# Kernel optimization log

Hardware: AMD Instinct MI355X
Metric: run time of the kernel (lower is better)

Reference implementation:

```python
import jax, jax.numpy as jnp
import numpy as np

B, N, E, S, HOPS, OD = 32, 325, 64, 12, 3, 1


def setup_inputs() -> dict:
    key = jax.random.key(0)
    ks = jax.random.split(key, 16)
    rn = lambda k, sh: jax.random.normal(k, sh, dtype=jnp.float32)
    return {
        "hidden": rn(ks[0], (B, N, E)),
        "supports": jax.random.uniform(ks[1], (2, N, N), dtype=jnp.float32),
        "target": rn(ks[2], (B, S, N, OD)),
        "memory": rn(ks[3], (HOPS + 1, B, N, E)),
        "nodevec1": rn(ks[4], (N, E)),
        "nodevec2": rn(ks[5], (N, E)),
        "gru_w_ih": rn(ks[6], (3 * E, OD)) * 0.1,
        "gru_w_hh": rn(ks[7], (3 * E, E)) * 0.1,
        "gru_b_ih": rn(ks[8], (3 * E,)) * 0.1,
        "gru_b_hh": rn(ks[9], (3 * E,)) * 0.1,
        "sent_w": rn(ks[10], (HOPS, E, E)) * 0.1,  # sentinel Linear (no bias), stored pre-transposed
        "bn_gamma": jnp.ones((HOPS, N), dtype=jnp.float32),
        "bn_beta": jnp.zeros((HOPS, N), dtype=jnp.float32),
        "gconv_w": rn(ks[11], (HOPS, 7 * E, E)) * 0.05,  # order*support_len+1 = 7 chunks
        "gconv_b": rn(ks[12], (HOPS, E)) * 0.05,
        "out_w": rn(ks[13], (E, OD)) * 0.1,
        "out_b": rn(ks[14], (OD,)) * 0.1,
    }


def _bn(x, gamma, beta, eps=1e-5):
    # nn.BatchNorm1d(num_nodes) on (B, N, E): channel dim is N, stats over (B, E) (training-mode batch stats)
    mean = x.mean(axis=(0, 2), keepdims=True)
    var = x.var(axis=(0, 2), keepdims=True)
    return (x - mean) / jnp.sqrt(var + eps) * gamma[None, :, None] + beta[None, :, None]


def _gconv(x, sup_list, score, W, b):
    # order=2, support_len=3 -> 1 + 2*3 = 7 concatenated chunks, then Linear(7E -> E)
    outs = [x]
    for adj in sup_list:
        x1 = jnp.einsum('nm,bme->bne', adj, x)
        outs.append(jnp.einsum('bnm,bme->bne', score, x1))
        x2 = jnp.einsum('nm,bme->bne', adj, x1)
        outs.append(jnp.einsum('bnm,bme->bne', score, x2))
    return jnp.concatenate(outs, axis=-1) @ W + b


def reference(hidden, supports, target, memory, nodevec1, nodevec2,
              gru_w_ih, gru_w_hh, gru_b_ih, gru_b_hh, sent_w,
              bn_gamma, bn_beta, gconv_w, gconv_b, out_w, out_b):
    Bn, Nn, Ee = hidden.shape
    scale = Ee ** 0.5
    adp = jax.nn.softmax(jax.nn.relu(nodevec1 @ nodevec2.T), axis=-1)
    sup_list = [supports[0], supports[1], adp]

    def step(carry, _):
        h, prev = carry  # h: (B,N,E), prev: (B,N,OD) previous prediction (zeros at t=0)
        gi = prev.reshape(Bn * Nn, -1) @ gru_w_ih.T + gru_b_ih
        gh = h.reshape(Bn * Nn, Ee) @ gru_w_hh.T + gru_b_hh
        i_r, i_z, i_n = jnp.split(gi, 3, axis=-1)
        h_r, h_z, h_n = jnp.split(gh, 3, axis=-1)
        r = jax.nn.sigmoid(i_r + h_r)
        z = jax.nn.sigmoid(i_z + h_z)
        n = jnp.tanh(i_n + r * h_n)
        h_new = ((1.0 - z) * n + z * h.reshape(Bn * Nn, Ee)).reshape(Bn, Nn, Ee)
        u = h_new
        sents, mems = [], []
        for hop in range(HOPS):
            key_m = memory[hop]  # (B,N,E)
            energy = jnp.einsum('bne,bme->bnm', u, key_m) / scale  # (B,N,N)
            sent = jnp.sum(u * (key_m @ sent_w[hop]), axis=-1) / scale  # (B,N)
            sents.append(sent)
            score = jax.nn.softmax(energy, axis=-1)
            o = _bn(_gconv(memory[hop + 1], sup_list, score, gconv_w[hop], gconv_b[hop]),
                    bn_gamma[hop], bn_beta[hop])
            mems.append(o)
            u = u + o
        sents = jnp.stack(sents, axis=-1)   # (B,N,hops)
        mems = jnp.stack(mems, axis=-2)     # (B,N,hops,E)
        # NOTE: original code weights with RAW sentinel energies, not sentinel_score (dead code) -- kept faithful
        out = jnp.sum(sents[..., None] * mems, axis=-2) @ out_w + out_b  # (B,N,OD)
        return (h_new, out), out

    init_out = jnp.zeros((Bn, Nn, OD), dtype=hidden.dtype)
    _, outs = jax.lax.scan(step, (hidden, init_out), None, length=S)  # (S,B,N,OD)
    return jnp.transpose(outs, (1, 0, 2, 3))  # (B,S,N,OD)
```

## Files before the change

### kernel.cpp

```cpp
#include <hip/hip_runtime.h>

constexpr int B = 32, N = 325, E = 64, S = 12, HOPS = 3;
constexpr int BN  = B * N;
constexpr int BNE = B * N * E;
constexpr int RT  = 16;
constexpr int NRT = (N + RT - 1) / RT;
constexpr int EP  = E + 4;
constexpr int NP  = 328;
constexpr int PSTR = 348;
constexpr int PBSTR = 360;
constexpr float SCALE_INV = 0.125f;

typedef __attribute__((ext_vector_type(8))) short short8v;
typedef __attribute__((ext_vector_type(4))) float f32x4;

__device__ inline short f2bf(float f) {
  unsigned x = __builtin_bit_cast(unsigned, f);
  return (short)((x + 0x7FFFu + ((x >> 16) & 1u)) >> 16);
}
__device__ inline float bf2f(short h) {
  unsigned x = ((unsigned)(unsigned short)h) << 16;
  return __builtin_bit_cast(float, x);
}

__global__ __launch_bounds__(256) void adp_kernel(const float* __restrict__ nv1,
                                                  const float* __restrict__ nv2,
                                                  float* __restrict__ adp) {
  int n = blockIdx.x;
  __shared__ float row[E];
  __shared__ float buf[N];
  __shared__ float red[256];
  int tid = threadIdx.x;
  if (tid < E) row[tid] = nv1[n * E + tid];
  __syncthreads();
  float lmax = -1e30f;
  for (int m = tid; m < N; m += 256) {
    const float* v2 = nv2 + (size_t)m * E;
    float s = 0.f;
#pragma unroll
    for (int e = 0; e < E; ++e) s += row[e] * v2[e];
    s = fmaxf(s, 0.f);
    buf[m] = s;
    lmax = fmaxf(lmax, s);
  }
  red[tid] = lmax;
  __syncthreads();
  for (int off = 128; off > 0; off >>= 1) {
    if (tid < off) red[tid] = fmaxf(red[tid], red[tid + off]);
    __syncthreads();
  }
  float mx = red[0];
  __syncthreads();
  float lsum = 0.f;
  for (int m = tid; m < N; m += 256) {
    float ev = expf(buf[m] - mx);
    buf[m] = ev;
    lsum += ev;
  }
  red[tid] = lsum;
  __syncthreads();
  for (int off = 128; off > 0; off >>= 1) {
    if (tid < off) red[tid] += red[tid + off];
    __syncthreads();
  }
  float inv = 1.f / red[0];
  for (int m = tid; m < N; m += 256) adp[(size_t)n * N + m] = buf[m] * inv;
}

__device__ inline void rowmm_body(const float* __restrict__ in, const float* __restrict__ W,
                                  const float* __restrict__ bias, float* __restrict__ out,
                                  int accum, int blk, int nblk) {
  __shared__ float Wl[E][E + 1];
  __shared__ float rbuf[4][4][E];
  int tid = threadIdx.x, w = tid >> 6, l = tid & 63;
  for (int idx = tid; idx < E * E; idx += 256) Wl[idx >> 6][idx & 63] = W[idx];
  __syncthreads();
  float bv = bias ? bias[l] : 0.f;
  constexpr int NG = BN / 16;
  for (int g = blk; g < NG; g += nblk) {
    int base = g * 16 + w * 4;
#pragma unroll
    for (int rr = 0; rr < 4; ++rr) rbuf[w][rr][l] = in[(size_t)(base + rr) * E + l];
    float acc[4];
#pragma unroll
    for (int rr = 0; rr < 4; ++rr)
      acc[rr] = accum ? out[(size_t)(base + rr) * E + l] : bv;
#pragma unroll
    for (int k = 0; k < 16; ++k) {
      float w0 = Wl[4 * k][l], w1 = Wl[4 * k + 1][l], w2 = Wl[4 * k + 2][l], w3 = Wl[4 * k + 3][l];
#pragma unroll
      for (int rr = 0; rr < 4; ++rr) {
        float4 rv = *(const float4*)&rbuf[w][rr][4 * k];
        acc[rr] += rv.x * w0 + rv.y * w1 + rv.z * w2 + rv.w * w3;
      }
    }
#pragma unroll
    for (int rr = 0; rr < 4; ++rr) out[(size_t)(base + rr) * E + l] = acc[rr];
  }
}

__global__ __launch_bounds__(256) void rowmmA_kernel(const float* __restrict__ memory,
                                                     const float* __restrict__ sent_w,
                                                     const float* __restrict__ gw,
                                                     const float* __restrict__ gb,
                                                     float* __restrict__ kms,
                                                     float* __restrict__ C0) {
  int c = blockIdx.x / 112, blk = blockIdx.x % 112;
  const float *in, *W, *bias;
  float* out;
  if (c < 3) {
    in = memory + (size_t)c * BNE; W = sent_w + (size_t)c * E * E; bias = nullptr;
    out = kms + (size_t)c * BNE;
  } else {
    int h = c - 3;
    in = memory + (size_t)(h + 1) * BNE; W = gw + (size_t)h * 7 * E * E; bias = gb + h * E;
    out = C0 + (size_t)h * BNE;
  }
  rowmm_body(in, W, bias, out, 0, blk, 112);
}

__global__ __launch_bounds__(256) void rowmmZ_kernel(const float* __restrict__ tbase,
                                                     const float* __restrict__ gw,
                                                     int chunk, float* __restrict__ Zb,
                                                     int accum) {
  int h = blockIdx.x / 224, blk = blockIdx.x % 224;
  rowmm_body(tbase + (size_t)h * BNE, gw + (size_t)h * 7 * E * E + (size_t)chunk * E * E,
             nullptr, Zb + (size_t)h * BNE, accum, blk, 224);
}

__global__ __launch_bounds__(256) void bmmB_kernel(const float* __restrict__ A,
                                                   const float* __restrict__ Xbase,
                                                   float* __restrict__ outBase) {
  int c = blockIdx.x / (B * NRT), rem = blockIdx.x % (B * NRT);
  int b = rem / NRT, rt = rem % NRT;
  const float* X = Xbase + (size_t)c * BNE;
  float* out = outBase + (size_t)c * BNE;
  int n0 = rt * RT, nrows = min(RT, N - n0);
  __shared__ float Ar[RT][NP];
  __shared__ float tile[64][EP];
  int tid = threadIdx.x, w = tid >> 6, l = tid & 63;
  for (int r = w; r < RT; r += 4)
    for (int m = l; m < NP; m += 64)
      Ar[r][m] = (r < nrows && m < N) ? A[(size_t)(n0 + r) * N + m] : 0.f;
  int ti = tid >> 2, c0 = (tid & 3) * 16;
  float acc[4] = {0.f, 0.f, 0.f, 0.f};
  for (int mt = 0; mt < 6; ++mt) {
    int m0 = mt * 64, mv = min(64, N - m0);
    __syncthreads();
    {
      float4 z0, z1, z2, z3;
      if (ti < mv) {
        const float4* src = (const float4*)(X + ((size_t)b * N + m0 + ti) * E + c0);
        z0 = src[0]; z1 = src[1]; z2 = src[2]; z3 = src[3];
      } else {
        z0 = z1 = z2 = z3 = make_float4(0.f, 0.f, 0.f, 0.f);
      }
      float4* dst = (float4*)&tile[ti][c0];
      dst[0] = z0; dst[1] = z1; dst[2] = z2; dst[3] = z3;
    }
    __syncthreads();
    int jmax = (mv + 3) >> 2;
#pragma unroll 4
    for (int j = 0; j < jmax; ++j) {
      float t0 = tile[4 * j][l], t1 = tile[4 * j + 1][l];
      float t2 = tile[4 * j + 2][l], t3 = tile[4 * j + 3][l];
#pragma unroll
      for (int rr = 0; rr < 4; ++rr) {
        float4 p = *(const float4*)&Ar[w * 4 + rr][m0 + 4 * j];
        acc[rr] += p.x * t0 + p.y * t1 + p.z * t2 + p.w * t3;
      }
    }
  }
#pragma unroll
  for (int rr = 0; rr < 4; ++rr) {
    int r = w * 4 + rr;
    if (r < nrows) out[((size_t)b * N + n0 + r) * E + l] = acc[rr];
  }
}

__global__ __launch_bounds__(128) void kpack_kernel(const float* __restrict__ memory,
                                                    short* __restrict__ kp) {
  int idx = blockIdx.x;
  int ct = idx % 21, hb = idx / 21;
  int tid = threadIdx.x, ks = tid >> 6, l = tid & 63;
  int m = ct * 16 + (l & 15);
  int e0 = ks * 32 + (l >> 4) * 8;
  short8v hi, lo;
  if (m < N) {
    const float* p = memory + ((size_t)hb * N + m) * E + e0;
#pragma unroll
    for (int j = 0; j < 8; ++j) {
      float f = p[j];
      short h = f2bf(f);
      hi[j] = h;
      lo[j] = f2bf(f - bf2f(h));
    }
  } else {
#pragma unroll
    for (int j = 0; j < 8; ++j) { hi[j] = 0; lo[j] = 0; }
  }
  size_t base = ((size_t)idx * 2 + ks) * 1024 + (size_t)l * 8;
  *(short8v*)(kp + base) = hi;
  *(short8v*)(kp + base + 512) = lo;
}

__global__ __launch_bounds__(64) void zpack_kernel(const float* __restrict__ Zb,
                                                   short* __restrict__ zp) {
  int idx = blockIdx.x;
  int et = idx & 3, hb = idx >> 2;
  int l = threadIdx.x;
  int e = et * 16 + (l & 15);
  int mbase = (l >> 4) * 8;
  const float* Zp = Zb + (size_t)hb * N * E;
  for (int ks = 0; ks < 11; ++ks) {
    short8v hi, lo;
#pragma unroll
    for (int j = 0; j < 8; ++j) {
      int m = ks * 32 + mbase + j;
      float f = (m < N) ? Zp[(size_t)m * E + e] : 0.f;
      short h = f2bf(f);
      hi[j] = h;
      lo[j] = f2bf(f - bf2f(h));
    }
    size_t base = ((size_t)idx * 11 + ks) * 1024 + (size_t)l * 8;
    *(short8v*)(zp + base) = hi;
    *(short8v*)(zp + base + 512) = lo;
  }
}

__global__ __launch_bounds__(256) void attn_kernel(
    const float* __restrict__ uPrev, const float* __restrict__ gprePrev,
    const float* __restrict__ statsPrev, const float* __restrict__ gammaPrev,
    const float* __restrict__ betaPrev, const float* __restrict__ outw,
    float* __restrict__ uOut, float* __restrict__ owPrev,
    const float* __restrict__ kms, const short* __restrict__ kp,
    const short* __restrict__ zp, const float* __restrict__ C0,
    float* __restrict__ gpre, float* __restrict__ statsCur,
    float* __restrict__ sent) {
  int b = blockIdx.x / 11, rt = blockIdx.x % 11;
  int n0 = rt * 32, nrows = min(32, N - n0);
  int tid = threadIdx.x, w = tid >> 6, l = tid & 63;
  __shared__ float uT[32][68];
  __shared__ float prob[32][PSTR];
  __shared__ short pb[32][PBSTR];
  __shared__ float rsum[32];
  size_t rowbase = (size_t)b * N + n0;

  for (int rr = 0; rr < 8; ++rr) {
    int r = w * 8 + rr;
    if (r < nrows) {
      size_t gi = (rowbase + r) * E + l;
      float uv;
      if (gprePrev) {
        int n = n0 + r;
        float m = statsPrev[n] * (1.f / 2048.f);
        float var = statsPrev[N + n] * (1.f / 2048.f) - m * m;
        float rstd = rsqrtf(var + 1e-5f);
        float o = (gprePrev[gi] - m) * rstd * gammaPrev[n] + betaPrev[n];
        uv = uPrev[gi] + o;
        if (uOut) uOut[gi] = uv;
        float tt = o * outw[l];
#pragma unroll
        for (int off = 32; off; off >>= 1) tt += __shfl_xor(tt, off);
        if (l == 0) owPrev[rowbase + r] = tt;
      } else {
        uv = uPrev[gi];
      }
      uT[r][l] = uv;
    } else if (r < 32) uT[r][l] = 0.f;
  }
  __syncthreads();
  for (int rr = 0; rr < 8; ++rr) {
    int r = w * 8 + rr;
    if (r < nrows) {
      float v = uT[r][l] * kms[(rowbase + r) * E + l];
#pragma unroll
      for (int off = 32; off; off >>= 1) v += __shfl_xor(v, off);
      if (l == 0) sent[rowbase + r] = v * SCALE_INV;
    }
  }
  short8v ah[2][2], al[2][2];
  {
    int arow = l & 15, ak = (l >> 4) * 8;
#pragma unroll
    for (int mt = 0; mt < 2; ++mt)
#pragma unroll
      for (int ks = 0; ks < 2; ++ks) {
        const float* p = &uT[mt * 16 + arow][ks * 32 + ak];
        short8v h, lo;
#pragma unroll
        for (int j = 0; j < 8; ++j) {
          float f = p[j];
          short hh = f2bf(f);
          h[j] = hh;
          lo[j] = f2bf(f - bf2f(hh));
        }
        ah[mt][ks] = h; al[mt][ks] = lo;
      }
  }
  const short8v* kpb = (const short8v*)(kp + (size_t)b * 21 * 2048);
  for (int ct = w; ct < 21; ct += 4) {
    short8v bh0 = kpb[(ct * 4 + 0) * 64 + l];
    short8v bl0 = kpb[(ct * 4 + 1) * 64 + l];
    short8v bh1 = kpb[(ct * 4 + 2) * 64 + l];
    short8v bl1 = kpb[(ct * 4 + 3) * 64 + l];
    f32x4 acc0 = {0.f, 0.f, 0.f, 0.f}, acc1 = {0.f, 0.f, 0.f, 0.f};
    acc0 = __builtin_amdgcn_mfma_f32_16x16x32_bf16(ah[0][0], bh0, acc0, 0, 0, 0);
    acc0 = __builtin_amdgcn_mfma_f32_16x16x32_bf16(ah[0][0], bl0, acc0, 0, 0, 0);
    acc0 = __builtin_amdgcn_mfma_f32_16x16x32_bf16(al[0][0], bh0, acc0, 0, 0, 0);
    acc0 = __builtin_amdgcn_mfma_f32_16x16x32_bf16(ah[0][1], bh1, acc0, 0, 0, 0);
    acc0 = __builtin_amdgcn_mfma_f32_16x16x32_bf16(ah[0][1], bl1, acc0, 0, 0, 0);
    acc0 = __builtin_amdgcn_mfma_f32_16x16x32_bf16(al[0][1], bh1, acc0, 0, 0, 0);
    acc1 = __builtin_amdgcn_mfma_f32_16x16x32_bf16(ah[1][0], bh0, acc1, 0, 0, 0);
    acc1 = __builtin_amdgcn_mfma_f32_16x16x32_bf16(ah[1][0], bl0, acc1, 0, 0, 0);
    acc1 = __builtin_amdgcn_mfma_f32_16x16x32_bf16(al[1][0], bh0, acc1, 0, 0, 0);
    acc1 = __builtin_amdgcn_mfma_f32_16x16x32_bf16(ah[1][1], bh1, acc1, 0, 0, 0);
    acc1 = __builtin_amdgcn_mfma_f32_16x16x32_bf16(ah[1][1], bl1, acc1, 0, 0, 0);
    acc1 = __builtin_amdgcn_mfma_f32_16x16x32_bf16(al[1][1], bh1, acc1, 0, 0, 0);
    int col = ct * 16 + (l & 15), r0 = (l >> 4) * 4;
#pragma unroll
    for (int r = 0; r < 4; ++r) {
      prob[r0 + r][col] = acc0[r] * SCALE_INV;
      prob[16 + r0 + r][col] = acc1[r] * SCALE_INV;
    }
  }
  __syncthreads();
  for (int rr = 0; rr < 8; ++rr) {
    int r = w * 8 + rr;
    if (r < nrows) {
      float v[6], mx = -1e30f;
#pragma unroll
      for (int k = 0; k < 6; ++k) {
        int m = l + 64 * k;
        v[k] = (m < N) ? prob[r][m] : -1e30f;
        mx = fmaxf(mx, v[k]);
      }
#pragma unroll
      for (int off = 32; off; off >>= 1) mx = fmaxf(mx, __shfl_xor(mx, off));
      float s = 0.f;
#pragma unroll
      for (int k = 0; k < 6; ++k) {
        int m = l + 64 * k;
        if (m < PBSTR) {
          if (m < N) {
            short pv = f2bf(expf(v[k] - mx));
            pb[r][m] = pv;
            s += bf2f(pv);
          } else {
            pb[r][m] = 0;
          }
        }
      }
#pragma unroll
      for (int off = 32; off; off >>= 1) s += __shfl_xor(s, off);
      if (l == 0) rsum[r] = s;
    }
  }
  __syncthreads();
  int mt = w >> 1, e2 = (w & 1) * 2;
  const short8v* zpb = (const short8v*)(zp + (size_t)b * 4 * 11 * 1024);
  f32x4 accA = {0.f, 0.f, 0.f, 0.f}, accB = {0.f, 0.f, 0.f, 0.f};
  {
    int arow = mt * 16 + (l & 15), ak = (l >> 4) * 8;
#pragma unroll
    for (int ks = 0; ks < 11; ++ks) {
      short8v a = *(const short8v*)&pb[arow][ks * 32 + ak];
      short8v zAh = zpb[((e2 * 11 + ks) * 2 + 0) * 64 + l];
      short8v zAl = zpb[((e2 * 11 + ks) * 2 + 1) * 64 + l];
      short8v zBh = zpb[(((e2 + 1) * 11 + ks) * 2 + 0) * 64 + l];
      short8v zBl = zpb[(((e2 + 1) * 11 + ks) * 2 + 1) * 64 + l];
      accA = __builtin_amdgcn_mfma_f32_16x16x32_bf16(a, zAh, accA, 0, 0, 0);
      accA = __builtin_amdgcn_mfma_f32_16x16x32_bf16(a, zAl, accA, 0, 0, 0);
      accB = __builtin_amdgcn_mfma_f32_16x16x32_bf16(a, zBh, accB, 0, 0, 0);
      accB = __builtin_amdgcn_mfma_f32_16x16x32_bf16(a, zBl, accB, 0, 0, 0);
    }
  }
  int r0 = (l >> 4) * 4, colA = e2 * 16 + (l & 15);
#pragma unroll
  for (int r = 0; r < 4; ++r) {
    int row = mt * 16 + r0 + r;
    if (row < nrows) {
      float inv = 1.f / rsum[row];
      size_t gi = (rowbase + row) * E;
      float gA = accA[r] * inv + C0[gi + colA];
      float gB = accB[r] * inv + C0[gi + colA + 16];
      gpre[gi + colA] = gA;
      gpre[gi + colA + 16] = gB;
      prob[row][colA] = gA;
      prob[row][colA + 16] = gB;
    }
  }
  __syncthreads();
  for (int rr = 0; rr < 8; ++rr) {
    int r = w * 8 + rr;
    if (r < nrows) {
      float v = prob[r][l];
      float s = v, q = v * v;
#pragma unroll
      for (int off = 32; off; off >>= 1) { s += __shfl_xor(s, off); q += __shfl_xor(q, off); }
      if (l == 0) {
        atomicAdd(&statsCur[n0 + r], s);
        atomicAdd(&statsCur[N + n0 + r], q);
      }
    }
  }
}

__global__ __launch_bounds__(256) void gru_kernel(float* __restrict__ h,
                                                  const float* __restrict__ prev,
                                                  const float* __restrict__ wih,
                                                  const float* __restrict__ whh,
                                                  const float* __restrict__ bih,
                                                  const float* __restrict__ bhh,
                                                  float* __restrict__ u) {
  __shared__ float W[3 * E][EP];
  __shared__ float hrow[4][E];
  int tid = threadIdx.x, w = tid >> 6, l = tid & 63;
  for (int idx = tid; idx < 3 * E * E; idx += 256) W[idx >> 6][idx & 63] = whh[idx];
  __syncthreads();
  float wi0 = wih[l], wi1 = wih[64 + l], wi2 = wih[128 + l];
  float bi0 = bih[l], bi1 = bih[64 + l], bi2 = bih[128 + l];
  float bh0 = bhh[l], bh1 = bhh[64 + l], bh2 = bhh[128 + l];
  int nw = gridDim.x * 4, wid = blockIdx.x * 4 + w;
  for (int row = wid; row < BN; row += nw) {
    float hv = h[(size_t)row * E + l];
    hrow[w][l] = hv;
    float g0 = bh0, g1 = bh1, g2 = bh2;
#pragma unroll
    for (int k = 0; k < 16; ++k) {
      float4 hh = *(const float4*)&hrow[w][4 * k];
      float4 a = *(const float4*)&W[l][4 * k];
      float4 bq = *(const float4*)&W[64 + l][4 * k];
      float4 c = *(const float4*)&W[128 + l][4 * k];
      g0 += hh.x * a.x + hh.y * a.y + hh.z * a.z + hh.w * a.w;
      g1 += hh.x * bq.x + hh.y * bq.y + hh.z * bq.z + hh.w * bq.w;
      g2 += hh.x * c.x + hh.y * c.y + hh.z * c.z + hh.w * c.w;
    }
    float pv = prev[row];
    float i0 = pv * wi0 + bi0;
    float i1 = pv * wi1 + bi1;
    float i2 = pv * wi2 + bi2;
    float r = 1.f / (1.f + expf(-(i0 + g0)));
    float z = 1.f / (1.f + expf(-(i1 + g1)));
    float nn = tanhf(i2 + r * g2);
    float hn = (1.f - z) * nn + z * hv;
    h[(size_t)row * E + l] = hn;
    u[(size_t)row * E + l] = hn;
  }
}

__global__ __launch_bounds__(256) void finish_kernel(
    const float* __restrict__ gpre2, const float* __restrict__ stats2,
    const float* __restrict__ gamma2, const float* __restrict__ beta2,
    const float* __restrict__ outw, const float* __restrict__ outb,
    const float* __restrict__ sent, const float* __restrict__ ow01,
    float* __restrict__ dout, float* __restrict__ prev, int t) {
  int tid = threadIdx.x, w = tid >> 6, l = tid & 63;
  int wid = blockIdx.x * 4 + w, nw = gridDim.x * 4;
  float wv = outw[l];
  for (int row = wid; row < BN; row += nw) {
    int n = row % N;
    float m = stats2[n] * (1.f / 2048.f);
    float var = stats2[N + n] * (1.f / 2048.f) - m * m;
    float rstd = rsqrtf(var + 1e-5f);
    float o = (gpre2[(size_t)row * E + l] - m) * rstd * gamma2[n] + beta2[n];
    float tt = o * wv;
#pragma unroll
    for (int off = 32; off; off >>= 1) tt += __shfl_xor(tt, off);
    if (l == 0) {
      float v = outb[0] + sent[row] * ow01[row] + sent[BN + row] * ow01[BN + row]
              + sent[2 * BN + row] * tt;
      int b = row / N;
      dout[((size_t)b * S + t) * N + (row - b * N)] = v;
      prev[row] = v;
    }
  }
}

extern "C" void kernel_launch(void* const* d_in, const int* in_sizes, int n_in,
                              void* d_out, int out_size, void* d_ws, size_t ws_size,
                              hipStream_t stream) {
  const float* hidden   = (const float*)d_in[0];
  const float* supports = (const float*)d_in[1];
  const float* memory   = (const float*)d_in[3];
  const float* nv1      = (const float*)d_in[4];
  const float* nv2      = (const float*)d_in[5];
  const float* wih      = (const float*)d_in[6];
  const float* whh      = (const float*)d_in[7];
  const float* bih      = (const float*)d_in[8];
  const float* bhh      = (const float*)d_in[9];
  const float* sent_w   = (const float*)d_in[10];
  const float* gamma    = (const float*)d_in[11];
  const float* beta     = (const float*)d_in[12];
  const float* gw       = (const float*)d_in[13];
  const float* gb       = (const float*)d_in[14];
  const float* outw     = (const float*)d_in[15];
  const float* outb     = (const float*)d_in[16];
  float* out = (float*)d_out;
  float* ws  = (float*)d_ws;

  size_t o = 0;
  float* adp   = ws + o; o += 105632;
  float* kms   = ws + o; o += (size_t)3 * BNE;
  float* C0b   = ws + o; o += (size_t)3 * BNE;
  float* hbuf  = ws + o; o += (size_t)BNE;
  float* ubuf  = ws + o; o += (size_t)BNE;
  float* u1    = ws + o; o += (size_t)BNE;
  float* uni   = ws + o; o += (size_t)9 * BNE;
  float* Zb  = uni;
  float* t1b = uni + (size_t)3 * BNE;
  float* t2b = uni + (size_t)6 * BNE;
  float* g0 = uni, *g1 = uni + BNE, *g2 = uni + (size_t)2 * BNE;
  short* kpackS = (short*)(ws + o); o += 2064384;
  short* zpackS = (short*)(ws + o); o += 2162688;
  float* prev   = ws + o; o += BN;
  float* sentb  = ws + o; o += (size_t)3 * BN;
  float* owb    = ws + o; o += (size_t)2 * BN;
  float* statsb = ws + o; o += (size_t)36 * 650;

  hipMemcpyAsync(hbuf, hidden, sizeof(float) * BNE, hipMemcpyDeviceToDevice, stream);
  hipMemsetAsync(prev, 0, sizeof(float) * BN, stream);
  hipMemsetAsync(statsb, 0, sizeof(float) * 36 * 650, stream);

  adp_kernel<<<N, 256, 0, stream>>>(nv1, nv2, adp);
  rowmmA_kernel<<<672, 256, 0, stream>>>(memory, sent_w, gw, gb, kms, C0b);
  kpack_kernel<<<3 * B * 21, 128, 0, stream>>>(memory, kpackS);

  for (int a = 0; a < 3; ++a) {
    const float* A = (a == 0) ? supports : (a == 1) ? supports + (size_t)N * N : adp;
    bmmB_kernel<<<3 * B * NRT, 256, 0, stream>>>(A, memory + BNE, t1b);
    rowmmZ_kernel<<<672, 256, 0, stream>>>(t1b, gw, 2 * a + 1, Zb, (a > 0) ? 1 : 0);
    bmmB_kernel<<<3 * B * NRT, 256, 0, stream>>>(A, t1b, t2b);
    rowmmZ_kernel<<<672, 256, 0, stream>>>(t2b, gw, 2 * a + 2, Zb, 1);
  }
  zpack_kernel<<<3 * B * 4, 64, 0, stream>>>(Zb, zpackS);

  for (int t = 0; t < S; ++t) {
    float* st0 = statsb + (size_t)(t * 3 + 0) * 650;
    float* st1 = statsb + (size_t)(t * 3 + 1) * 650;
    float* st2 = statsb + (size_t)(t * 3 + 2) * 650;
    gru_kernel<<<512, 256, 0, stream>>>(hbuf, prev, wih, whh, bih, bhh, ubuf);
    attn_kernel<<<B * 11, 256, 0, stream>>>(
        ubuf, nullptr, nullptr, nullptr, nullptr, outw, nullptr, nullptr,
        kms, kpackS, zpackS, C0b, g0, st0, sentb);
    attn_kernel<<<B * 11, 256, 0, stream>>>(
        ubuf, g0, st0, gamma, beta, outw, u1, owb,
        kms + BNE, kpackS + (size_t)B * 21 * 2048, zpackS + (size_t)B * 4 * 11 * 1024,
        C0b + BNE, g1, st1, sentb + BN);
    attn_kernel<<<B * 11, 256, 0, stream>>>(
        u1, g1, st1, gamma + N, beta + N, outw, nullptr, owb + BN,
        kms + (size_t)2 * BNE, kpackS + (size_t)2 * B * 21 * 2048,
        zpackS + (size_t)2 * B * 4 * 11 * 1024,
        C0b + (size_t)2 * BNE, g2, st2, sentb + (size_t)2 * BN);
    finish_kernel<<<256, 256, 0, stream>>>(g2, st2, gamma + 2 * N, beta + 2 * N,
                                           outw, outb, sentb, owb, out, prev, t);
  }
}
```

Before: 2.436 ms.

## Keep attention scores in registers, widen attn blocks, fuse finish into GRU

The attention kernel now runs 512 threads (8 waves) per block. Each wave keeps its QK^T score tiles in registers and does the softmax max and sum through shuffles plus a small shared-memory reduction, so the float prob buffer in shared memory goes away. The PV matmul is split so each wave computes one 16x16 output tile, and the batch-norm statistics are reduced with shuffles in the epilogue. The per-step finish kernel is folded into the next step's GRU kernel, which computes the previous output directly and drops the prev buffer; only one finish launch remains after the loop. This removes launches and shared-memory traffic, at the cost of more cross-wave synchronisation and more register pressure.

```diff
diff --git a/kernel.cpp b/kernel.cpp
--- a/kernel.cpp
+++ b/kernel.cpp
@@ -7,7 +7,6 @@
 constexpr int NRT = (N + RT - 1) / RT;
 constexpr int EP  = E + 4;
 constexpr int NP  = 328;
-constexpr int PSTR = 348;
 constexpr int PBSTR = 360;
 constexpr float SCALE_INV = 0.125f;
 
@@ -228,7 +227,7 @@
   }
 }
 
-__global__ __launch_bounds__(256) void attn_kernel(
+__global__ __launch_bounds__(512) void attn_kernel(
     const float* __restrict__ uPrev, const float* __restrict__ gprePrev,
     const float* __restrict__ statsPrev, const float* __restrict__ gammaPrev,
     const float* __restrict__ betaPrev, const float* __restrict__ outw,
@@ -241,13 +240,20 @@
   int n0 = rt * 32, nrows = min(32, N - n0);
   int tid = threadIdx.x, w = tid >> 6, l = tid & 63;
   __shared__ float uT[32][68];
-  __shared__ float prob[32][PSTR];
   __shared__ short pb[32][PBSTR];
-  __shared__ float rsum[32];
+  __shared__ float rowred[32][8];
+  __shared__ float rmax[32];
+  __shared__ float rsinv[32];
   size_t rowbase = (size_t)b * N + n0;
-
-  for (int rr = 0; rr < 8; ++rr) {
-    int r = w * 8 + rr;
+  int g = l >> 4;
+
+  for (int idx = tid; idx < 32 * (PBSTR - 336); idx += 512) {
+    int r = idx / (PBSTR - 336), c = idx - r * (PBSTR - 336);
+    pb[r][336 + c] = 0;
+  }
+#pragma unroll
+  for (int rr = 0; rr < 4; ++rr) {
+    int r = w * 4 + rr;
     if (r < nrows) {
       size_t gi = (rowbase + r) * E + l;
       float uv;
@@ -267,11 +273,14 @@
         uv = uPrev[gi];
       }
       uT[r][l] = uv;
-    } else if (r < 32) uT[r][l] = 0.f;
-  }
-  __syncthreads();
-  for (int rr = 0; rr < 8; ++rr) {
-    int r = w * 8 + rr;
+    } else {
+      uT[r][l] = 0.f;
+    }
+  }
+  __syncthreads();
+#pragma unroll
+  for (int rr = 0; rr < 4; ++rr) {
+    int r = w * 4 + rr;
     if (r < nrows) {
       float v = uT[r][l] * kms[(rowbase + r) * E + l];
 #pragma unroll
@@ -281,7 +290,7 @@
   }
   short8v ah[2][2], al[2][2];
   {
-    int arow = l & 15, ak = (l >> 4) * 8;
+    int arow = l & 15, ak = g * 8;
 #pragma unroll
     for (int mt = 0; mt < 2; ++mt)
 #pragma unroll
@@ -299,120 +308,162 @@
       }
   }
   const short8v* kpb = (const short8v*)(kp + (size_t)b * 21 * 2048);
-  for (int ct = w; ct < 21; ct += 4) {
-    short8v bh0 = kpb[(ct * 4 + 0) * 64 + l];
-    short8v bl0 = kpb[(ct * 4 + 1) * 64 + l];
-    short8v bh1 = kpb[(ct * 4 + 2) * 64 + l];
-    short8v bl1 = kpb[(ct * 4 + 3) * 64 + l];
-    f32x4 acc0 = {0.f, 0.f, 0.f, 0.f}, acc1 = {0.f, 0.f, 0.f, 0.f};
-    acc0 = __builtin_amdgcn_mfma_f32_16x16x32_bf16(ah[0][0], bh0, acc0, 0, 0, 0);
-    acc0 = __builtin_amdgcn_mfma_f32_16x16x32_bf16(ah[0][0], bl0, acc0, 0, 0, 0);
-    acc0 = __builtin_amdgcn_mfma_f32_16x16x32_bf16(al[0][0], bh0, acc0, 0, 0, 0);
-    acc0 = __builtin_amdgcn_mfma_f32_16x16x32_bf16(ah[0][1], bh1, acc0, 0, 0, 0);
-    acc0 = __builtin_amdgcn_mfma_f32_16x16x32_bf16(ah[0][1], bl1, acc0, 0, 0, 0);
-    acc0 = __builtin_amdgcn_mfma_f32_16x16x32_bf16(al[0][1], bh1, acc0, 0, 0, 0);
-    acc1 = __builtin_amdgcn_mfma_f32_16x16x32_bf16(ah[1][0], bh0, acc1, 0, 0, 0);
-    acc1 = __builtin_amdgcn_mfma_f32_16x16x32_bf16(ah[1][0], bl0, acc1, 0, 0, 0);
-    acc1 = __builtin_amdgcn_mfma_f32_16x16x32_bf16(al[1][0], bh0, acc1, 0, 0, 0);
-    acc1 = __builtin_amdgcn_mfma_f32_16x16x32_bf16(ah[1][1], bh1, acc1, 0, 0, 0);
-    acc1 = __builtin_amdgcn_mfma_f32_16x16x32_bf16(ah[1][1], bl1, acc1, 0, 0, 0);
-    acc1 = __builtin_amdgcn_mfma_f32_16x16x32_bf16(al[1][1], bh1, acc1, 0, 0, 0);
-    int col = ct * 16 + (l & 15), r0 = (l >> 4) * 4;
+  f32x4 acc0[3], acc1[3];
+#pragma unroll
+  for (int i = 0; i < 3; ++i) {
+    acc0[i] = (f32x4){0.f, 0.f, 0.f, 0.f};
+    acc1[i] = (f32x4){0.f, 0.f, 0.f, 0.f};
+    int ct = w + 8 * i;
+    if (ct < 21) {
+      short8v bh0 = kpb[(ct * 4 + 0) * 64 + l];
+      short8v bl0 = kpb[(ct * 4 + 1) * 64 + l];
+      short8v bh1 = kpb[(ct * 4 + 2) * 64 + l];
+      short8v bl1 = kpb[(ct * 4 + 3) * 64 + l];
+      f32x4 a0 = acc0[i], a1 = acc1[i];
+      a0 = __builtin_amdgcn_mfma_f32_16x16x32_bf16(ah[0][0], bh0, a0, 0, 0, 0);
+      a0 = __builtin_amdgcn_mfma_f32_16x16x32_bf16(ah[0][0], bl0, a0, 0, 0, 0);
+      a0 = __builtin_amdgcn_mfma_f32_16x16x32_bf16(al[0][0], bh0, a0, 0, 0, 0);
+      a0 = __builtin_amdgcn_mfma_f32_16x16x32_bf16(ah[0][1], bh1, a0, 0, 0, 0);
+      a0 = __builtin_amdgcn_mfma_f32_16x16x32_bf16(ah[0][1], bl1, a0, 0, 0, 0);
+      a0 = __builtin_amdgcn_mfma_f32_16x16x32_bf16(al[0][1], bh1, a0, 0, 0, 0);
+      a1 = __builtin_amdgcn_mfma_f32_16x16x32_bf16(ah[1][0], bh0, a1, 0, 0, 0);
+      a1 = __builtin_amdgcn_mfma_f32_16x16x32_bf16(ah[1][0], bl0, a1, 0, 0, 0);
+      a1 = __builtin_amdgcn_mfma_f32_16x16x32_bf16(al[1][0], bh0, a1, 0, 0, 0);
+      a1 = __builtin_amdgcn_mfma_f32_16x16x32_bf16(ah[1][1], bh1, a1, 0, 0, 0);
+      a1 = __builtin_amdgcn_mfma_f32_16x16x32_bf16(ah[1][1], bl1, a1, 0, 0, 0);
+      a1 = __builtin_amdgcn_mfma_f32_16x16x32_bf16(al[1][1], bh1, a1, 0, 0, 0);
+      acc0[i] = a0; acc1[i] = a1;
+    }
+  }
+  {
+    float m0[4], m1[4];
 #pragma unroll
     for (int r = 0; r < 4; ++r) {
-      prob[r0 + r][col] = acc0[r] * SCALE_INV;
-      prob[16 + r0 + r][col] = acc1[r] * SCALE_INV;
-    }
-  }
-  __syncthreads();
-  for (int rr = 0; rr < 8; ++rr) {
-    int r = w * 8 + rr;
-    if (r < nrows) {
-      float v[6], mx = -1e30f;
-#pragma unroll
-      for (int k = 0; k < 6; ++k) {
-        int m = l + 64 * k;
-        v[k] = (m < N) ? prob[r][m] : -1e30f;
-        mx = fmaxf(mx, v[k]);
-      }
-#pragma unroll
-      for (int off = 32; off; off >>= 1) mx = fmaxf(mx, __shfl_xor(mx, off));
-      float s = 0.f;
-#pragma unroll
-      for (int k = 0; k < 6; ++k) {
-        int m = l + 64 * k;
-        if (m < PBSTR) {
-          if (m < N) {
-            short pv = f2bf(expf(v[k] - mx));
-            pb[r][m] = pv;
-            s += bf2f(pv);
-          } else {
-            pb[r][m] = 0;
+      float a = -1e30f, c = -1e30f;
+#pragma unroll
+      for (int i = 0; i < 3; ++i)
+        if (w + 8 * i < 21) { a = fmaxf(a, acc0[i][r]); c = fmaxf(c, acc1[i][r]); }
+#pragma unroll
+      for (int off = 1; off < 16; off <<= 1) {
+        a = fmaxf(a, __shfl_xor(a, off));
+        c = fmaxf(c, __shfl_xor(c, off));
+      }
+      m0[r] = a; m1[r] = c;
+    }
+    if ((l & 15) == 0) {
+#pragma unroll
+      for (int r = 0; r < 4; ++r) {
+        rowred[g * 4 + r][w] = m0[r];
+        rowred[16 + g * 4 + r][w] = m1[r];
+      }
+    }
+  }
+  __syncthreads();
+  if (tid < 32) {
+    float a = rowred[tid][0];
+#pragma unroll
+    for (int j = 1; j < 8; ++j) a = fmaxf(a, rowred[tid][j]);
+    rmax[tid] = a;
+  }
+  __syncthreads();
+  {
+    float mx0[4], mx1[4], s0[4], s1[4];
+#pragma unroll
+    for (int r = 0; r < 4; ++r) {
+      mx0[r] = rmax[g * 4 + r]; mx1[r] = rmax[16 + g * 4 + r];
+      s0[r] = 0.f; s1[r] = 0.f;
+    }
+#pragma unroll
+    for (int i = 0; i < 3; ++i) {
+      int ct = w + 8 * i;
+      if (ct < 21) {
+        int col = ct * 16 + (l & 15);
+        bool valid = col < N;
+#pragma unroll
+        for (int r = 0; r < 4; ++r) {
+          short pv0 = 0, pv1 = 0;
+          if (valid) {
+            pv0 = f2bf(expf((acc0[i][r] - mx0[r]) * SCALE_INV));
+            pv1 = f2bf(expf((acc1[i][r] - mx1[r]) * SCALE_INV));
+            s0[r] += bf2f(pv0);
+            s1[r] += bf2f(pv1);
           }
+          pb[g * 4 + r][col] = pv0;
+          pb[16 + g * 4 + r][col] = pv1;
         }
       }
-#pragma unroll
-      for (int off = 32; off; off >>= 1) s += __shfl_xor(s, off);
-      if (l == 0) rsum[r] = s;
-    }
-  }
-  __syncthreads();
-  int mt = w >> 1, e2 = (w & 1) * 2;
+    }
+#pragma unroll
+    for (int r = 0; r < 4; ++r) {
+#pragma unroll
+      for (int off = 1; off < 16; off <<= 1) {
+        s0[r] += __shfl_xor(s0[r], off);
+        s1[r] += __shfl_xor(s1[r], off);
+      }
+    }
+    if ((l & 15) == 0) {
+#pragma unroll
+      for (int r = 0; r < 4; ++r) {
+        rowred[g * 4 + r][w] = s0[r];
+        rowred[16 + g * 4 + r][w] = s1[r];
+      }
+    }
+  }
+  __syncthreads();
+  if (tid < 32) {
+    float s = 0.f;
+#pragma unroll
+    for (int j = 0; j < 8; ++j) s += rowred[tid][j];
+    rsinv[tid] = 1.f / s;
+  }
+  __syncthreads();
+  int mt = w >> 2, et = w & 3;
   const short8v* zpb = (const short8v*)(zp + (size_t)b * 4 * 11 * 1024);
-  f32x4 accA = {0.f, 0.f, 0.f, 0.f}, accB = {0.f, 0.f, 0.f, 0.f};
+  f32x4 acc = {0.f, 0.f, 0.f, 0.f};
   {
-    int arow = mt * 16 + (l & 15), ak = (l >> 4) * 8;
+    int arow = mt * 16 + (l & 15), ak = g * 8;
 #pragma unroll
     for (int ks = 0; ks < 11; ++ks) {
       short8v a = *(const short8v*)&pb[arow][ks * 32 + ak];
-      short8v zAh = zpb[((e2 * 11 + ks) * 2 + 0) * 64 + l];
-      short8v zAl = zpb[((e2 * 11 + ks) * 2 + 1) * 64 + l];
-      short8v zBh = zpb[(((e2 + 1) * 11 + ks) * 2 + 0) * 64 + l];
-      short8v zBl = zpb[(((e2 + 1) * 11 + ks) * 2 + 1) * 64 + l];
-      accA = __builtin_amdgcn_mfma_f32_16x16x32_bf16(a, zAh, accA, 0, 0, 0);
-      accA = __builtin_amdgcn_mfma_f32_16x16x32_bf16(a, zAl, accA, 0, 0, 0);
-      accB = __builtin_amdgcn_mfma_f32_16x16x32_bf16(a, zBh, accB, 0, 0, 0);
-      accB = __builtin_amdgcn_mfma_f32_16x16x32_bf16(a, zBl, accB, 0, 0, 0);
-    }
-  }
-  int r0 = (l >> 4) * 4, colA = e2 * 16 + (l & 15);
+      short8v zh = zpb[((et * 11 + ks) * 2 + 0) * 64 + l];
+      short8v zl = zpb[((et * 11 + ks) * 2 + 1) * 64 + l];
+      acc = __builtin_amdgcn_mfma_f32_16x16x32_bf16(a, zh, acc, 0, 0, 0);
+      acc = __builtin_amdgcn_mfma_f32_16x16x32_bf16(a, zl, acc, 0, 0, 0);
+    }
+  }
+  int colA = et * 16 + (l & 15);
 #pragma unroll
   for (int r = 0; r < 4; ++r) {
-    int row = mt * 16 + r0 + r;
+    int row = mt * 16 + g * 4 + r;
+    float sval = 0.f, qval = 0.f;
     if (row < nrows) {
-      float inv = 1.f / rsum[row];
-      size_t gi = (rowbase + row) * E;
-      float gA = accA[r] * inv + C0[gi + colA];
-      float gB = accB[r] * inv + C0[gi + colA + 16];
-      gpre[gi + colA] = gA;
-      gpre[gi + colA + 16] = gB;
-      prob[row][colA] = gA;
-      prob[row][colA + 16] = gB;
-    }
-  }
-  __syncthreads();
-  for (int rr = 0; rr < 8; ++rr) {
-    int r = w * 8 + rr;
-    if (r < nrows) {
-      float v = prob[r][l];
-      float s = v, q = v * v;
-#pragma unroll
-      for (int off = 32; off; off >>= 1) { s += __shfl_xor(s, off); q += __shfl_xor(q, off); }
-      if (l == 0) {
-        atomicAdd(&statsCur[n0 + r], s);
-        atomicAdd(&statsCur[N + n0 + r], q);
-      }
-    }
-  }
-}
-
-__global__ __launch_bounds__(256) void gru_kernel(float* __restrict__ h,
-                                                  const float* __restrict__ prev,
-                                                  const float* __restrict__ wih,
-                                                  const float* __restrict__ whh,
-                                                  const float* __restrict__ bih,
-                                                  const float* __restrict__ bhh,
-                                                  float* __restrict__ u) {
+      size_t gi = (rowbase + row) * E + colA;
+      float gA = acc[r] * rsinv[row] + C0[gi];
+      gpre[gi] = gA;
+      sval = gA; qval = gA * gA;
+    }
+#pragma unroll
+    for (int off = 1; off < 16; off <<= 1) {
+      sval += __shfl_xor(sval, off);
+      qval += __shfl_xor(qval, off);
+    }
+    if ((l & 15) == 0 && row < nrows) {
+      atomicAdd(&statsCur[n0 + row], sval);
+      atomicAdd(&statsCur[N + n0 + row], qval);
+    }
+  }
+}
+
+__global__ __launch_bounds__(256) void gru_kernel(
+    float* __restrict__ h,
+    const float* __restrict__ gpre2, const float* __restrict__ stats2,
+    const float* __restrict__ gamma2, const float* __restrict__ beta2,
+    const float* __restrict__ outw, const float* __restrict__ outb,
+    const float* __restrict__ sentb, const float* __restrict__ owb,
+    float* __restrict__ dout, int tprev,
+    const float* __restrict__ wih, const float* __restrict__ whh,
+    const float* __restrict__ bih, const float* __restrict__ bhh,
+    float* __restrict__ u) {
   __shared__ float W[3 * E][EP];
   __shared__ float hrow[4][E];
   int tid = threadIdx.x, w = tid >> 6, l = tid & 63;
@@ -421,10 +472,30 @@
   float wi0 = wih[l], wi1 = wih[64 + l], wi2 = wih[128 + l];
   float bi0 = bih[l], bi1 = bih[64 + l], bi2 = bih[128 + l];
   float bh0 = bhh[l], bh1 = bhh[64 + l], bh2 = bhh[128 + l];
+  float wv = outw[l];
+  float ob = outb[0];
   int nw = gridDim.x * 4, wid = blockIdx.x * 4 + w;
   for (int row = wid; row < BN; row += nw) {
     float hv = h[(size_t)row * E + l];
     hrow[w][l] = hv;
+    float pv = 0.f;
+    if (gpre2) {
+      int n = row % N;
+      float m = stats2[n] * (1.f / 2048.f);
+      float var = stats2[N + n] * (1.f / 2048.f) - m * m;
+      float rstd = rsqrtf(var + 1e-5f);
+      float o = (gpre2[(size_t)row * E + l] - m) * rstd * gamma2[n] + beta2[n];
+      float tt = o * wv;
+#pragma unroll
+      for (int off = 32; off; off >>= 1) tt += __shfl_xor(tt, off);
+      float v = ob + sentb[row] * owb[row] + sentb[BN + row] * owb[BN + row]
+              + sentb[2 * BN + row] * tt;
+      pv = v;
+      if (l == 0) {
+        int bb = row / N;
+        dout[((size_t)bb * S + tprev) * N + (row - bb * N)] = v;
+      }
+    }
     float g0 = bh0, g1 = bh1, g2 = bh2;
 #pragma unroll
     for (int k = 0; k < 16; ++k) {
@@ -436,7 +507,6 @@
       g1 += hh.x * bq.x + hh.y * bq.y + hh.z * bq.z + hh.w * bq.w;
       g2 += hh.x * c.x + hh.y * c.y + hh.z * c.z + hh.w * c.w;
     }
-    float pv = prev[row];
     float i0 = pv * wi0 + bi0;
     float i1 = pv * wi1 + bi1;
     float i2 = pv * wi2 + bi2;
@@ -454,7 +524,7 @@
     const float* __restrict__ gamma2, const float* __restrict__ beta2,
     const float* __restrict__ outw, const float* __restrict__ outb,
     const float* __restrict__ sent, const float* __restrict__ ow01,
-    float* __restrict__ dout, float* __restrict__ prev, int t) {
+    float* __restrict__ dout, int t) {
   int tid = threadIdx.x, w = tid >> 6, l = tid & 63;
   int wid = blockIdx.x * 4 + w, nw = gridDim.x * 4;
   float wv = outw[l];
@@ -472,7 +542,6 @@
               + sent[2 * BN + row] * tt;
       int b = row / N;
       dout[((size_t)b * S + t) * N + (row - b * N)] = v;
-      prev[row] = v;
     }
   }
 }
@@ -513,13 +582,11 @@
   float* g0 = uni, *g1 = uni + BNE, *g2 = uni + (size_t)2 * BNE;
   short* kpackS = (short*)(ws + o); o += 2064384;
   short* zpackS = (short*)(ws + o); o += 2162688;
-  float* prev   = ws + o; o += BN;
   float* sentb  = ws + o; o += (size_t)3 * BN;
   float* owb    = ws + o; o += (size_t)2 * BN;
   float* statsb = ws + o; o += (size_t)36 * 650;
 
   hipMemcpyAsync(hbuf, hidden, sizeof(float) * BNE, hipMemcpyDeviceToDevice, stream);
-  hipMemsetAsync(prev, 0, sizeof(float) * BN, stream);
   hipMemsetAsync(statsb, 0, sizeof(float) * 36 * 650, stream);
 
   adp_kernel<<<N, 256, 0, stream>>>(nv1, nv2, adp);
@@ -539,20 +606,25 @@
     float* st0 = statsb + (size_t)(t * 3 + 0) * 650;
     float* st1 = statsb + (size_t)(t * 3 + 1) * 650;
     float* st2 = statsb + (size_t)(t * 3 + 2) * 650;
-    gru_kernel<<<512, 256, 0, stream>>>(hbuf, prev, wih, whh, bih, bhh, ubuf);
-    attn_kernel<<<B * 11, 256, 0, stream>>>(
+    const float* g2prev  = (t == 0) ? nullptr : g2;
+    const float* st2prev = (t == 0) ? nullptr : statsb + (size_t)((t - 1) * 3 + 2) * 650;
+    gru_kernel<<<512, 256, 0, stream>>>(hbuf, g2prev, st2prev, gamma + 2 * N, beta + 2 * N,
+                                        outw, outb, sentb, owb, out, t - 1,
+                                        wih, whh, bih, bhh, ubuf);
+    attn_kernel<<<B * 11, 512, 0, stream>>>(
         ubuf, nullptr, nullptr, nullptr, nullptr, outw, nullptr, nullptr,
         kms, kpackS, zpackS, C0b, g0, st0, sentb);
-    attn_kernel<<<B * 11, 256, 0, stream>>>(
+    attn_kernel<<<B * 11, 512, 0, stream>>>(
         ubuf, g0, st0, gamma, beta, outw, u1, owb,
         kms + BNE, kpackS + (size_t)B * 21 * 2048, zpackS + (size_t)B * 4 * 11 * 1024,
         C0b + BNE, g1, st1, sentb + BN);
-    attn_kernel<<<B * 11, 256, 0, stream>>>(
+    attn_kernel<<<B * 11, 512, 0, stream>>>(
         u1, g1, st1, gamma + N, beta + N, outw, nullptr, owb + BN,
         kms + (size_t)2 * BNE, kpackS + (size_t)2 * B * 21 * 2048,
         zpackS + (size_t)2 * B * 4 * 11 * 1024,
         C0b + (size_t)2 * BNE, g2, st2, sentb + (size_t)2 * BN);
-    finish_kernel<<<256, 256, 0, stream>>>(g2, st2, gamma + 2 * N, beta + 2 * N,
-                                           outw, outb, sentb, owb, out, prev, t);
-  }
-}
+  }
+  finish_kernel<<<256, 256, 0, stream>>>(g2, statsb + (size_t)(11 * 3 + 2) * 650,
+                                         gamma + 2 * N, beta + 2 * N,
+                                         outw, outb, sentb, owb, out, S - 1);
+}
```

Result: faster. 2.304 ms (-5.4%).
